# Kernel optimization log

Hardware: AMD Instinct MI355X
Metric: run time of the kernel (lower is better)

The kernel has to match this reference:

```python
import jax, jax.numpy as jnp
import numpy as np


def _apply_rope(x, cos, sin):
    # x: [B, h, T, d]; cos/sin: [T, d//2]
    B, h, T, d = x.shape
    xp = x.astype(jnp.float32).reshape(B, h, T, d // 2, 2)
    xr, xi = xp[..., 0], xp[..., 1]
    c = cos[None, None]  # [1,1,T,d//2]
    s = sin[None, None]
    out_r = xr * c - xi * s
    out_i = xr * s + xi * c
    out = jnp.stack([out_r, out_i], axis=-1).reshape(B, h, T, d)
    return out.astype(x.dtype)


def setup_inputs() -> dict:
    key = jax.random.key(0)
    ks = jax.random.split(key, 7)
    B, T, C = 1, 4096, 1024
    h = 16
    d = C // h
    return {
        "x": jax.random.normal(ks[0], (B, T, C), jnp.float32),
        "freqs_cos": jax.random.normal(ks[1], (T, d // 2), jnp.float32),
        "freqs_sin": jax.random.normal(ks[2], (T, d // 2), jnp.float32),
        "Wq": jax.random.normal(ks[3], (C, C), jnp.float32) * 0.02,
        "Wk": jax.random.normal(ks[4], (C, C), jnp.float32) * 0.02,
        "Wv": jax.random.normal(ks[5], (C, C), jnp.float32) * 0.02,
        "Wo": jax.random.normal(ks[6], (C, C), jnp.float32) * 0.02,
    }


def reference(x, freqs_cos, freqs_sin, Wq, Wk, Wv, Wo):
    B, T, C = x.shape
    h = 16
    d = C // h
    # nn.Linear(bias=False): y = x @ W^T, W is [out, in]
    q = jnp.einsum("btc,oc->bto", x, Wq).reshape(B, T, h, d).transpose(0, 2, 1, 3)
    k = jnp.einsum("btc,oc->bto", x, Wk).reshape(B, T, h, d).transpose(0, 2, 1, 3)
    v = jnp.einsum("btc,oc->bto", x, Wv).reshape(B, T, h, d).transpose(0, 2, 1, 3)
    q = _apply_rope(q, freqs_cos, freqs_sin)
    k = _apply_rope(k, freqs_cos, freqs_sin)
    scale = 1.0 / jnp.sqrt(jnp.asarray(d, x.dtype))
    scores = jnp.einsum("bhqd,bhkd->bhqk", q, k) * scale  # [B,h,T,T]
    causal = jnp.tril(jnp.ones((T, T), bool))
    scores = jnp.where(causal[None, None], scores, -jnp.inf)
    att = jax.nn.softmax(scores.astype(jnp.float32), axis=-1).astype(q.dtype)
    y = jnp.einsum("bhqk,bhkd->bhqd", att, v)
    y = y.transpose(0, 2, 1, 3).reshape(B, T, C)
    return jnp.einsum("btc,oc->bto", y, Wo)  # dropout p=0 (eval)
```

## Files before the change

### kernel.cpp

```cpp
#include <hip/hip_runtime.h>
#include <hip/hip_bf16.h>
#include <math.h>

#define TT 4096
#define CC 1024
#define NH 16
#define HD 64

typedef unsigned short ushortT;
typedef __attribute__((ext_vector_type(8))) short short8;
typedef __attribute__((ext_vector_type(4))) float f32x4;

#define GLOAD_LDS16(gp, lp)                                                   \
    __builtin_amdgcn_global_load_lds(                                         \
        (const __attribute__((address_space(1))) void*)(gp),                  \
        (__attribute__((address_space(3))) void*)(lp), 16, 0, 0)

#define EXP2F(x) __builtin_amdgcn_exp2f(x)

__device__ __forceinline__ ushortT f2bf(float f) {
    __hip_bfloat16 h = __float2bfloat16(f);
    ushortT u; __builtin_memcpy(&u, &h, 2); return u;
}
__device__ __forceinline__ float bf2f(ushortT u) {
    return __uint_as_float(((unsigned)u) << 16);
}

#define PSLOT_BYTES 17408
#define NCHUNK_H 62
#define NTICK (NCHUNK_H * NH)

__global__ __launch_bounds__(256) void cvt_all(
    const float* __restrict__ x,  const float* __restrict__ wq,
    const float* __restrict__ wk, const float* __restrict__ wv,
    const float* __restrict__ wo,
    ushortT* __restrict__ xb,  ushortT* __restrict__ wqb,
    ushortT* __restrict__ wkb, ushortT* __restrict__ wvb,
    ushortT* __restrict__ wob)
{
    const int i = (blockIdx.x * 256 + threadIdx.x) * 4;
    const int NX = TT * CC, NW = CC * CC;
    const float* s; ushortT* d; int off;
    if (i < NX)               { s = x;  d = xb;  off = i; }
    else if (i < NX + NW)     { s = wq; d = wqb; off = i - NX; }
    else if (i < NX + 2 * NW) { s = wk; d = wkb; off = i - NX - NW; }
    else if (i < NX + 3 * NW) { s = wv; d = wvb; off = i - NX - 2 * NW; }
    else                      { s = wo; d = wob; off = i - NX - 3 * NW; }
    float4 v = *(const float4*)(s + off);
    *(ushort4*)(d + off) = make_ushort4(f2bf(v.x), f2bf(v.y), f2bf(v.z), f2bf(v.w));
}

__global__ __launch_bounds__(256) void gemm_qkv(
    const ushortT* __restrict__ A,
    const ushortT* __restrict__ Bq, const ushortT* __restrict__ Bk,
    const ushortT* __restrict__ Bv,
    const float* __restrict__ fcos, const float* __restrict__ fsin,
    ushortT* __restrict__ q16, ushortT* __restrict__ k16,
    ushortT* __restrict__ vt16)
{
    __shared__ char lds[49152];

    const int z = blockIdx.z;
    const ushortT* B = (z == 0) ? Bq : (z == 1) ? Bk : Bv;

    const int lin = (int)(blockIdx.y * gridDim.x + blockIdx.x);
    const int nwg8 = (int)((gridDim.x * gridDim.y) >> 3);
    const int swz = (lin & 7) * nwg8 + (lin >> 3);
    const int bm = (swz % (int)gridDim.x) * 128;
    const int bn = (swz / (int)gridDim.x) * 128;
    const int tid = threadIdx.x;
    const int w = tid >> 6, l = tid & 63;
    const int wm = w >> 1, wn = w & 1;

    f32x4 acc[4][4] = {};

    auto stageg = [&](int kk, int base) {
        #pragma unroll
        for (int e = 0; e < 2; ++e) {
            const int D = (w * 2 + e) * 1024 + l * 16;
            const int r = D >> 6;
            const int c = (D & 63) >> 1;
            GLOAD_LDS16(A + (size_t)(bm + r) * CC + kk + c, lds + base + (w * 2 + e) * 1024);
            GLOAD_LDS16(B + (size_t)(bn + r) * CC + kk + c, lds + base + 8192 + (w * 2 + e) * 1024);
        }
    };

    stageg(0, 0);
    stageg(32, 16384);

    for (int kt = 0; kt < 32; ++kt) {
        const int cur = kt % 3;
        if (kt + 2 < 32) {
            stageg((kt + 2) * 32, ((kt + 2) % 3) * 16384);
            asm volatile("s_waitcnt vmcnt(8)" ::: "memory");
        } else if (kt + 1 < 32) {
            asm volatile("s_waitcnt vmcnt(4)" ::: "memory");
        } else {
            asm volatile("s_waitcnt vmcnt(0)" ::: "memory");
        }
        __builtin_amdgcn_s_barrier();
        __builtin_amdgcn_sched_barrier(0);

        const ushortT* As = (const ushortT*)(lds + cur * 16384);
        const ushortT* Bs = (const ushortT*)(lds + cur * 16384 + 8192);

        short8 af[4], bfr[4];
        #pragma unroll
        for (int i = 0; i < 4; ++i) {
            int row = wm * 64 + i * 16 + (l & 15);
            af[i] = *(const short8*)(As + row * 32 + (l >> 4) * 8);
        }
        #pragma unroll
        for (int j = 0; j < 4; ++j) {
            int row = wn * 64 + j * 16 + (l & 15);
            bfr[j] = *(const short8*)(Bs + row * 32 + (l >> 4) * 8);
        }
        #pragma unroll
        for (int i = 0; i < 4; ++i)
            #pragma unroll
            for (int j = 0; j < 4; ++j)
                acc[i][j] = __builtin_amdgcn_mfma_f32_16x16x32_bf16(af[i], bfr[j], acc[i][j], 0, 0, 0);
        __builtin_amdgcn_s_barrier();
    }

    if (z < 2) {
        const float rsc = (z == 0) ? 0.18033688011112042f : 1.0f;
        ushortT* dq = (z == 0) ? q16 : k16;
        float* cs = (float*)lds;
        float* sn = (float*)(lds + 16384);
        for (int idx = tid; idx < 128 * 32; idx += 256) {
            int rr = idx >> 5, cc2 = idx & 31;
            cs[idx] = fcos[(size_t)(bm + rr) * 32 + cc2];
            sn[idx] = fsin[(size_t)(bm + rr) * 32 + cc2];
        }
        __syncthreads();
        #pragma unroll
        for (int i = 0; i < 4; ++i)
            #pragma unroll
            for (int j = 0; j < 4; ++j)
                #pragma unroll
                for (int r = 0; r < 4; ++r) {
                    const int lt = wm * 64 + i * 16 + (l >> 4) * 4 + r;
                    const int o = bn + wn * 64 + j * 16 + (l & 15);
                    const float v = acc[i][j][r];
                    const float p = __shfl_xor(v, 1);
                    const int pp = (o & 63) >> 1;
                    const float cv = cs[lt * 32 + pp], sv = sn[lt * 32 + pp];
                    const float outv = ((o & 1) ? (p * sv + v * cv) : (v * cv - p * sv)) * rsc;
                    const int t = bm + lt, head = o >> 6, dd = o & 63;
                    dq[((size_t)head * TT + t) * HD + dd] = f2bf(outv);
                }
    } else {
        #pragma unroll
        for (int i = 0; i < 4; ++i)
            #pragma unroll
            for (int j = 0; j < 4; ++j)
                #pragma unroll
                for (int r = 0; r < 4; ++r) {
                    const int t = bm + wm * 64 + i * 16 + (l >> 4) * 4 + r;
                    const int o = bn + wn * 64 + j * 16 + (l & 15);
                    const int head = o >> 6, dd = o & 63;
                    const int k = t & 63;
                    const int slot = (k & 32) | (((k >> 2) & 3) << 3)
                                   | (((k >> 4) & 1) << 2) | (k & 3);
                    vt16[((size_t)(head * HD + dd)) * TT + (t & ~63) + slot] = f2bf(acc[i][j][r]);
                }
    }
}

__global__ __launch_bounds__(256) void gemm_out(
    const ushortT* __restrict__ A, const ushortT* __restrict__ B,
    float* __restrict__ dout)
{
    __shared__ char lds[49152];

    const int lin = (int)(blockIdx.y * gridDim.x + blockIdx.x);
    const int nwg8 = (int)((gridDim.x * gridDim.y) >> 3);
    const int swz = (lin & 7) * nwg8 + (lin >> 3);
    const int bm = (swz % (int)gridDim.x) * 128;
    const int bn = (swz / (int)gridDim.x) * 128;
    const int tid = threadIdx.x;
    const int w = tid >> 6, l = tid & 63;
    const int wm = w >> 1, wn = w & 1;

    f32x4 acc[4][4] = {};

    auto stageg = [&](int kk, int base) {
        #pragma unroll
        for (int e = 0; e < 2; ++e) {
            const int D = (w * 2 + e) * 1024 + l * 16;
            const int r = D >> 6;
            const int c = (D & 63) >> 1;
            GLOAD_LDS16(A + (size_t)(bm + r) * CC + kk + c, lds + base + (w * 2 + e) * 1024);
            GLOAD_LDS16(B + (size_t)(bn + r) * CC + kk + c, lds + base + 8192 + (w * 2 + e) * 1024);
        }
    };

    stageg(0, 0);
    stageg(32, 16384);

    for (int kt = 0; kt < 32; ++kt) {
        const int cur = kt % 3;
        if (kt + 2 < 32) {
            stageg((kt + 2) * 32, ((kt + 2) % 3) * 16384);
            asm volatile("s_waitcnt vmcnt(8)" ::: "memory");
        } else if (kt + 1 < 32) {
            asm volatile("s_waitcnt vmcnt(4)" ::: "memory");
        } else {
            asm volatile("s_waitcnt vmcnt(0)" ::: "memory");
        }
        __builtin_amdgcn_s_barrier();
        __builtin_amdgcn_sched_barrier(0);

        const ushortT* As = (const ushortT*)(lds + cur * 16384);
        const ushortT* Bs = (const ushortT*)(lds + cur * 16384 + 8192);

        short8 af[4], bfr[4];
        #pragma unroll
        for (int i = 0; i < 4; ++i) {
            int row = wm * 64 + i * 16 + (l & 15);
            af[i] = *(const short8*)(As + row * 32 + (l >> 4) * 8);
        }
        #pragma unroll
        for (int j = 0; j < 4; ++j) {
            int row = wn * 64 + j * 16 + (l & 15);
            bfr[j] = *(const short8*)(Bs + row * 32 + (l >> 4) * 8);
        }
        #pragma unroll
        for (int i = 0; i < 4; ++i)
            #pragma unroll
            for (int j = 0; j < 4; ++j)
                acc[i][j] = __builtin_amdgcn_mfma_f32_16x16x32_bf16(af[i], bfr[j], acc[i][j], 0, 0, 0);
        __builtin_amdgcn_s_barrier();
    }

    #pragma unroll
    for (int i = 0; i < 4; ++i)
        #pragma unroll
        for (int j = 0; j < 4; ++j)
            #pragma unroll
            for (int r = 0; r < 4; ++r) {
                const int t = bm + wm * 64 + i * 16 + (l >> 4) * 4 + r;
                const int o = bn + wn * 64 + j * 16 + (l & 15);
                dout[(size_t)t * CC + o] = acc[i][j][r];
            }
}

__global__ __launch_bounds__(512) void attn_mfma(
    const ushortT* __restrict__ q16, const ushortT* __restrict__ k16,
    const ushortT* __restrict__ vt16, ushortT* __restrict__ y16,
    char* __restrict__ parts, int* __restrict__ counter)
{
    const int tid = threadIdx.x;
    const int w = tid >> 6, l = tid & 63;
    const int g = l >> 4, q = l & 15;

    __shared__ char lds[32768];

    for (;;) {
        if (tid == 0) {
            int tk0 = atomicAdd(counter, 1);
            *(int*)lds = tk0;
        }
        __syncthreads();
        const int tk = *(const int*)lds;
        __syncthreads();
        if (tk >= NTICK) break;

        const int head = tk / NCHUNK_H;
        const int t = tk - head * NCHUNK_H;
        int qc, ci, nsplit;
        if (t < 27)      { qc = 31 - t / 3; ci = t % 3; nsplit = 3; }
        else if (t < 51) { int u = t - 27; qc = 22 - u / 2; ci = u & 1; nsplit = 2; }
        else             { qc = 10 - (t - 51); ci = -1; nsplit = 1; }
        const int ntl = 2 * qc + 2;
        const int kb0 = (ci <= 0) ? 0 : ci * ntl / nsplit;
        const int kb1 = (ci < 0) ? (ntl - 1) : ((ci + 1) * ntl / nsplit - 1);

        const int rowbase = qc * 128 + w * 16;
        const int qrow = rowbase + q;
        short8 qa[2];
        {
            const ushortT* qp = q16 + ((size_t)head * TT + qrow) * HD + g * 8;
            qa[0] = *(const short8*)(qp);
            qa[1] = *(const short8*)(qp + 32);
        }

        f32x4 yacc[4] = {};
        float m_s = -1e30f, l_s = 0.0f;

        auto stage = [&](int kb, int base) {
            #pragma unroll
            for (int e = 0; e < 2; ++e) {
                const int seg = w * 2 + e;
                const int D = seg * 1024 + l * 16;
                if (seg < 8) {
                    const int row = D >> 7;
                    const int src = D ^ ((row & 7) << 4);
                    const int col = (src & 127) >> 1;
                    GLOAD_LDS16(k16 + ((size_t)head * TT + (size_t)kb * 64 + row) * HD + col,
                                lds + base + seg * 1024);
                } else {
                    const int Dv = D - 8192;
                    const int row = Dv >> 7;
                    const int src = Dv ^ ((row & 7) << 4);
                    const int col = (src & 127) >> 1;
                    GLOAD_LDS16(vt16 + ((size_t)head * HD + row) * TT + (size_t)kb * 64 + col,
                                lds + base + seg * 1024);
                }
            }
        };

        int cur = 0;
        stage(kb0, 0);

        for (int kb = kb0; kb <= kb1; ++kb) {
            if (kb + 1 <= kb1) {
                stage(kb + 1, (cur ^ 1) * 16384);
                asm volatile("s_waitcnt vmcnt(2)" ::: "memory");
            } else {
                asm volatile("s_waitcnt vmcnt(0)" ::: "memory");
            }
            __builtin_amdgcn_s_barrier();
            __builtin_amdgcn_sched_barrier(0);

            const bool skip = (kb * 64 > rowbase + 15);
            if (!skip) {
                const char* Ks  = lds + cur * 16384;
                const char* Vts = Ks + 8192;

                f32x4 s[4] = {};
                __builtin_amdgcn_s_setprio(1);
                #pragma unroll
                for (int ks = 0; ks < 2; ++ks)
                    #pragma unroll
                    for (int kg = 0; kg < 4; ++kg) {
                        const int key = kg * 16 + q;
                        int b = key * 128 + ks * 64 + g * 16;
                        b ^= (key & 7) << 4;
                        short8 kf = *(const short8*)(Ks + b);
                        s[kg] = __builtin_amdgcn_mfma_f32_16x16x32_bf16(kf, qa[ks], s[kg], 0, 0, 0);
                    }
                __builtin_amdgcn_s_setprio(0);

                if (kb * 64 + 63 > rowbase) {
                    #pragma unroll
                    for (int kg = 0; kg < 4; ++kg)
                        #pragma unroll
                        for (int r = 0; r < 4; ++r)
                            if (kb * 64 + kg * 16 + 4 * g + r > qrow) s[kg][r] = -1e30f;
                }

                float ilmax = s[0][0];
                #pragma unroll
                for (int kg = 0; kg < 4; ++kg)
                    #pragma unroll
                    for (int r = 0; r < 4; ++r)
                        ilmax = fmaxf(ilmax, s[kg][r]);

                if (__any(ilmax > m_s + 8.0f)) {
                    float mx = ilmax;
                    mx = fmaxf(mx, __shfl_xor(mx, 16));
                    mx = fmaxf(mx, __shfl_xor(mx, 32));
                    const float mnew = fmaxf(m_s, mx);
                    const float al = EXP2F(m_s - mnew);
                    m_s = mnew;
                    l_s *= al;
                    float aly[4];
                    #pragma unroll
                    for (int r = 0; r < 4; ++r)
                        aly[r] = __shfl(al, 20 * g + r);
                    #pragma unroll
                    for (int dg = 0; dg < 4; ++dg)
                        #pragma unroll
                        for (int r = 0; r < 4; ++r)
                            yacc[dg][r] *= aly[r];
                }

                unsigned U[4], V[4];
                float ls = 0.0f;
                #pragma unroll
                for (int kg = 0; kg < 4; ++kg) {
                    const float p0 = EXP2F(s[kg][0] - m_s);
                    const float p1 = EXP2F(s[kg][1] - m_s);
                    const float p2 = EXP2F(s[kg][2] - m_s);
                    const float p3 = EXP2F(s[kg][3] - m_s);
                    ls += (p0 + p1) + (p2 + p3);
                    asm("v_cvt_pk_bf16_f32 %0, %1, %2" : "=v"(U[kg]) : "v"(p0), "v"(p1));
                    asm("v_cvt_pk_bf16_f32 %0, %1, %2" : "=v"(V[kg]) : "v"(p2), "v"(p3));
                }
                l_s += ls;

                __builtin_amdgcn_s_setprio(1);
                #pragma unroll
                for (int ks2 = 0; ks2 < 2; ++ks2) {
                    union { unsigned u[4]; short8 s8; } pu;
                    pu.u[0] = U[2 * ks2];     pu.u[1] = V[2 * ks2];
                    pu.u[2] = U[2 * ks2 + 1]; pu.u[3] = V[2 * ks2 + 1];
                    const short8 pa = pu.s8;
                    const char* Vts2 = Vts;
                    #pragma unroll
                    for (int dg = 0; dg < 4; ++dg) {
                        const int dd = dg * 16 + q;
                        int vb = dd * 128 + ks2 * 64 + g * 16;
                        vb ^= (dd & 7) << 4;
                        short8 vf = *(const short8*)(Vts2 + vb);
                        yacc[dg] = __builtin_amdgcn_mfma_f32_16x16x32_bf16(pa, vf, yacc[dg], 0, 0, 0);
                    }
                }
                __builtin_amdgcn_s_setprio(0);
            }
            __builtin_amdgcn_s_barrier();
            cur ^= 1;
        }

        l_s += __shfl_xor(l_s, 16);
        l_s += __shfl_xor(l_s, 32);
        float lr[4];
        #pragma unroll
        for (int r = 0; r < 4; ++r)
            lr[r] = __shfl(l_s, 20 * g + r);

        if (ci < 0) {
            #pragma unroll
            for (int r = 0; r < 4; ++r) lr[r] = 1.0f / lr[r];
            #pragma unroll
            for (int dg = 0; dg < 4; ++dg)
                #pragma unroll
                for (int r = 0; r < 4; ++r) {
                    const int trow = rowbase + 4 * g + r;
                    const int col = head * HD + dg * 16 + q;
                    y16[(size_t)trow * CC + col] = f2bf(yacc[dg][r] * lr[r]);
                }
        } else {
            float mr[4];
            #pragma unroll
            for (int r = 0; r < 4; ++r)
                mr[r] = __shfl(m_s, 20 * g + r);
            const int sidx = head * 51 +
                ((qc >= 23) ? (31 - qc) * 3 + ci : 27 + (22 - qc) * 2 + ci);
            char* pb = parts + (size_t)sidx * PSLOT_BYTES;
            ushortT* yp = (ushortT*)pb;
            float* mp = (float*)(pb + 16384);
            float* lp = (float*)(pb + 16896);
            #pragma unroll
            for (int dg = 0; dg < 4; ++dg)
                #pragma unroll
                for (int r = 0; r < 4; ++r) {
                    const int row = w * 16 + 4 * g + r;
                    yp[row * 64 + dg * 16 + q] = f2bf(yacc[dg][r]);
                }
            if (q == 0) {
                #pragma unroll
                for (int r = 0; r < 4; ++r) {
                    const int row = w * 16 + 4 * g + r;
                    mp[row] = mr[r];
                    lp[row] = lr[r];
                }
            }
        }
    }
}

__global__ __launch_bounds__(256) void attn_combine(
    const char* __restrict__ parts, ushortT* __restrict__ y16)
{
    const int qc = 11 + blockIdx.x;
    const int head = blockIdx.y;
    const int nsplit = (qc >= 23) ? 3 : 2;
    const int base = head * 51 + ((qc >= 23) ? (31 - qc) * 3 : 27 + (22 - qc) * 2);
    const int tid = threadIdx.x;

    #pragma unroll
    for (int pass = 0; pass < 4; ++pass) {
        const int idx = pass * 2048 + tid * 8;
        const int row = idx >> 6, col = idx & 63;

        float m_i[3], l_i[3];
        float M = -1e30f;
        for (int i = 0; i < nsplit; ++i) {
            const char* pb = parts + (size_t)(base + i) * PSLOT_BYTES;
            m_i[i] = *(const float*)(pb + 16384 + row * 4);
            l_i[i] = *(const float*)(pb + 16896 + row * 4);
            M = fmaxf(M, m_i[i]);
        }
        float wgt[3], L = 0.0f;
        for (int i = 0; i < nsplit; ++i) {
            wgt[i] = EXP2F(m_i[i] - M);
            L += l_i[i] * wgt[i];
        }
        const float Linv = 1.0f / L;

        float acc[8] = {};
        for (int i = 0; i < nsplit; ++i) {
            const ushortT* yp = (const ushortT*)(parts + (size_t)(base + i) * PSLOT_BYTES);
            short8 v = *(const short8*)(yp + row * 64 + col);
            #pragma unroll
            for (int j = 0; j < 8; ++j)
                acc[j] += bf2f((ushortT)v[j]) * wgt[i];
        }
        union { ushortT u[8]; short8 s8; } ov;
        #pragma unroll
        for (int j = 0; j < 8; ++j)
            ov.u[j] = f2bf(acc[j] * Linv);
        const int trow = qc * 128 + row;
        *(short8*)(&y16[(size_t)trow * CC + head * HD + col]) = ov.s8;
    }
}

extern "C" void kernel_launch(void* const* d_in, const int* in_sizes, int n_in,
                              void* d_out, int out_size, void* d_ws, size_t ws_size,
                              hipStream_t stream) {
    const float* x    = (const float*)d_in[0];
    const float* fcos = (const float*)d_in[1];
    const float* fsin = (const float*)d_in[2];
    const float* Wq   = (const float*)d_in[3];
    const float* Wk   = (const float*)d_in[4];
    const float* Wv   = (const float*)d_in[5];
    const float* Wo   = (const float*)d_in[6];
    float* out = (float*)d_out;

    char* ws = (char*)d_ws;
    ushortT* xb  = (ushortT*)(ws);
    ushortT* wqb = (ushortT*)(ws + (8u << 20));
    ushortT* wkb = (ushortT*)(ws + (10u << 20));
    ushortT* wvb = (ushortT*)(ws + (12u << 20));
    ushortT* wob = (ushortT*)(ws + (14u << 20));
    ushortT* q16 = (ushortT*)(ws + (16u << 20));
    ushortT* k16 = (ushortT*)(ws + (24u << 20));
    ushortT* vt16 = (ushortT*)(ws + (32u << 20));
    ushortT* y16 = (ushortT*)(ws + (40u << 20));
    char* parts = ws;
    int* counter = (int*)(ws + (14u << 20) - 16);

    cvt_all<<<(TT * CC + 4 * CC * CC) / 4 / 256, 256, 0, stream>>>(
        x, Wq, Wk, Wv, Wo, xb, wqb, wkb, wvb, wob);

    dim3 qkvgrid(TT / 128, CC / 128, 3);
    gemm_qkv<<<qkvgrid, 256, 0, stream>>>(xb, wqb, wkb, wvb, fcos, fsin,
                                          q16, k16, vt16);

    hipMemsetAsync(counter, 0, 4, stream);
    attn_mfma<<<1024, 512, 0, stream>>>(q16, k16, vt16, y16, parts, counter);

    dim3 cgrid(21, NH);
    attn_combine<<<cgrid, 256, 0, stream>>>(parts, y16);

    dim3 ggrid(TT / 128, CC / 128);
    gemm_out<<<ggrid, 256, 0, stream>>>(y16, wob, out);
}
```

Measured before the change: 143.5 us.

## Process two 16-row query tiles per wave to reuse K/V fragments

```diff
diff --git a/kernel.cpp b/kernel.cpp
--- a/kernel.cpp
+++ b/kernel.cpp
@@ -246,7 +246,7 @@
             }
 }
 
-__global__ __launch_bounds__(512) void attn_mfma(
+__global__ __launch_bounds__(256) void attn_mfma(
     const ushortT* __restrict__ q16, const ushortT* __restrict__ k16,
     const ushortT* __restrict__ vt16, ushortT* __restrict__ y16,
     char* __restrict__ parts, int* __restrict__ counter)
@@ -277,22 +277,26 @@
         const int kb0 = (ci <= 0) ? 0 : ci * ntl / nsplit;
         const int kb1 = (ci < 0) ? (ntl - 1) : ((ci + 1) * ntl / nsplit - 1);
 
-        const int rowbase = qc * 128 + w * 16;
-        const int qrow = rowbase + q;
-        short8 qa[2];
+        const int rowbase = qc * 128 + w * 32;
+        const int qrowA = rowbase + q;
+        const int qrowB = rowbase + 16 + q;
+        short8 qaA[2], qaB[2];
         {
-            const ushortT* qp = q16 + ((size_t)head * TT + qrow) * HD + g * 8;
-            qa[0] = *(const short8*)(qp);
-            qa[1] = *(const short8*)(qp + 32);
-        }
-
-        f32x4 yacc[4] = {};
-        float m_s = -1e30f, l_s = 0.0f;
+            const ushortT* qp = q16 + ((size_t)head * TT + qrowA) * HD + g * 8;
+            qaA[0] = *(const short8*)(qp);
+            qaA[1] = *(const short8*)(qp + 32);
+            const ushortT* qp2 = q16 + ((size_t)head * TT + qrowB) * HD + g * 8;
+            qaB[0] = *(const short8*)(qp2);
+            qaB[1] = *(const short8*)(qp2 + 32);
+        }
+
+        f32x4 yA[4] = {}, yB[4] = {};
+        float mA = -1e30f, lA = 0.0f, mB = -1e30f, lB = 0.0f;
 
         auto stage = [&](int kb, int base) {
             #pragma unroll
-            for (int e = 0; e < 2; ++e) {
-                const int seg = w * 2 + e;
+            for (int e = 0; e < 4; ++e) {
+                const int seg = w * 4 + e;
                 const int D = seg * 1024 + l * 16;
                 if (seg < 8) {
                     const int row = D >> 7;
@@ -317,19 +321,19 @@
         for (int kb = kb0; kb <= kb1; ++kb) {
             if (kb + 1 <= kb1) {
                 stage(kb + 1, (cur ^ 1) * 16384);
-                asm volatile("s_waitcnt vmcnt(2)" ::: "memory");
+                asm volatile("s_waitcnt vmcnt(4)" ::: "memory");
             } else {
                 asm volatile("s_waitcnt vmcnt(0)" ::: "memory");
             }
             __builtin_amdgcn_s_barrier();
             __builtin_amdgcn_sched_barrier(0);
 
-            const bool skip = (kb * 64 > rowbase + 15);
+            const bool skip = (kb * 64 > rowbase + 31);
             if (!skip) {
                 const char* Ks  = lds + cur * 16384;
                 const char* Vts = Ks + 8192;
 
-                f32x4 s[4] = {};
+                f32x4 sA[4] = {}, sB[4] = {};
                 __builtin_amdgcn_s_setprio(1);
                 #pragma unroll
                 for (int ks = 0; ks < 2; ++ks)
@@ -338,8 +342,9 @@
                         const int key = kg * 16 + q;
                         int b = key * 128 + ks * 64 + g * 16;
                         b ^= (key & 7) << 4;
-                        short8 kf = *(const short8*)(Ks + b);
-                        s[kg] = __builtin_amdgcn_mfma_f32_16x16x32_bf16(kf, qa[ks], s[kg], 0, 0, 0);
+                        const short8 kf = *(const short8*)(Ks + b);
+                        sA[kg] = __builtin_amdgcn_mfma_f32_16x16x32_bf16(kf, qaA[ks], sA[kg], 0, 0, 0);
+                        sB[kg] = __builtin_amdgcn_mfma_f32_16x16x32_bf16(kf, qaB[ks], sB[kg], 0, 0, 0);
                     }
                 __builtin_amdgcn_s_setprio(0);
 
@@ -347,25 +352,27 @@
                     #pragma unroll
                     for (int kg = 0; kg < 4; ++kg)
                         #pragma unroll
-                        for (int r = 0; r < 4; ++r)
-                            if (kb * 64 + kg * 16 + 4 * g + r > qrow) s[kg][r] = -1e30f;
-                }
-
-                float ilmax = s[0][0];
+                        for (int r = 0; r < 4; ++r) {
+                            const int key = kb * 64 + kg * 16 + 4 * g + r;
+                            if (key > qrowA) sA[kg][r] = -1e30f;
+                            if (key > qrowB) sB[kg][r] = -1e30f;
+                        }
+                }
+
+                float ilmax = sA[0][0];
                 #pragma unroll
                 for (int kg = 0; kg < 4; ++kg)
                     #pragma unroll
                     for (int r = 0; r < 4; ++r)
-                        ilmax = fmaxf(ilmax, s[kg][r]);
-
-                if (__any(ilmax > m_s + 8.0f)) {
+                        ilmax = fmaxf(ilmax, sA[kg][r]);
+                if (__any(ilmax > mA + 8.0f)) {
                     float mx = ilmax;
                     mx = fmaxf(mx, __shfl_xor(mx, 16));
                     mx = fmaxf(mx, __shfl_xor(mx, 32));
-                    const float mnew = fmaxf(m_s, mx);
-                    const float al = EXP2F(m_s - mnew);
-                    m_s = mnew;
-                    l_s *= al;
+                    const float mnew = fmaxf(mA, mx);
+                    const float al = EXP2F(mA - mnew);
+                    mA = mnew;
+                    lA *= al;
                     float aly[4];
                     #pragma unroll
                     for (int r = 0; r < 4; ++r)
@@ -374,38 +381,80 @@
                     for (int dg = 0; dg < 4; ++dg)
                         #pragma unroll
                         for (int r = 0; r < 4; ++r)
-                            yacc[dg][r] *= aly[r];
-                }
-
-                unsigned U[4], V[4];
-                float ls = 0.0f;
-                #pragma unroll
-                for (int kg = 0; kg < 4; ++kg) {
-                    const float p0 = EXP2F(s[kg][0] - m_s);
-                    const float p1 = EXP2F(s[kg][1] - m_s);
-                    const float p2 = EXP2F(s[kg][2] - m_s);
-                    const float p3 = EXP2F(s[kg][3] - m_s);
-                    ls += (p0 + p1) + (p2 + p3);
-                    asm("v_cvt_pk_bf16_f32 %0, %1, %2" : "=v"(U[kg]) : "v"(p0), "v"(p1));
-                    asm("v_cvt_pk_bf16_f32 %0, %1, %2" : "=v"(V[kg]) : "v"(p2), "v"(p3));
-                }
-                l_s += ls;
+                            yA[dg][r] *= aly[r];
+                }
+                unsigned UA[4], VA[4];
+                {
+                    float ls = 0.0f;
+                    #pragma unroll
+                    for (int kg = 0; kg < 4; ++kg) {
+                        const float p0 = EXP2F(sA[kg][0] - mA);
+                        const float p1 = EXP2F(sA[kg][1] - mA);
+                        const float p2 = EXP2F(sA[kg][2] - mA);
+                        const float p3 = EXP2F(sA[kg][3] - mA);
+                        ls += (p0 + p1) + (p2 + p3);
+                        asm("v_cvt_pk_bf16_f32 %0, %1, %2" : "=v"(UA[kg]) : "v"(p0), "v"(p1));
+                        asm("v_cvt_pk_bf16_f32 %0, %1, %2" : "=v"(VA[kg]) : "v"(p2), "v"(p3));
+                    }
+                    lA += ls;
+                }
+
+                float ilmaxB = sB[0][0];
+                #pragma unroll
+                for (int kg = 0; kg < 4; ++kg)
+                    #pragma unroll
+                    for (int r = 0; r < 4; ++r)
+                        ilmaxB = fmaxf(ilmaxB, sB[kg][r]);
+                if (__any(ilmaxB > mB + 8.0f)) {
+                    float mx = ilmaxB;
+                    mx = fmaxf(mx, __shfl_xor(mx, 16));
+                    mx = fmaxf(mx, __shfl_xor(mx, 32));
+                    const float mnew = fmaxf(mB, mx);
+                    const float al = EXP2F(mB - mnew);
+                    mB = mnew;
+                    lB *= al;
+                    float aly[4];
+                    #pragma unroll
+                    for (int r = 0; r < 4; ++r)
+                        aly[r] = __shfl(al, 20 * g + r);
+                    #pragma unroll
+                    for (int dg = 0; dg < 4; ++dg)
+                        #pragma unroll
+                        for (int r = 0; r < 4; ++r)
+                            yB[dg][r] *= aly[r];
+                }
+                unsigned UB[4], VB[4];
+                {
+                    float ls = 0.0f;
+                    #pragma unroll
+                    for (int kg = 0; kg < 4; ++kg) {
+                        const float p0 = EXP2F(sB[kg][0] - mB);
+                        const float p1 = EXP2F(sB[kg][1] - mB);
+                        const float p2 = EXP2F(sB[kg][2] - mB);
+                        const float p3 = EXP2F(sB[kg][3] - mB);
+                        ls += (p0 + p1) + (p2 + p3);
+                        asm("v_cvt_pk_bf16_f32 %0, %1, %2" : "=v"(UB[kg]) : "v"(p0), "v"(p1));
+                        asm("v_cvt_pk_bf16_f32 %0, %1, %2" : "=v"(VB[kg]) : "v"(p2), "v"(p3));
+                    }
+                    lB += ls;
+                }
 
                 __builtin_amdgcn_s_setprio(1);
                 #pragma unroll
                 for (int ks2 = 0; ks2 < 2; ++ks2) {
-                    union { unsigned u[4]; short8 s8; } pu;
-                    pu.u[0] = U[2 * ks2];     pu.u[1] = V[2 * ks2];
-                    pu.u[2] = U[2 * ks2 + 1]; pu.u[3] = V[2 * ks2 + 1];
-                    const short8 pa = pu.s8;
-                    const char* Vts2 = Vts;
+                    union { unsigned u[4]; short8 s8; } pa, pb;
+                    pa.u[0] = UA[2 * ks2];     pa.u[1] = VA[2 * ks2];
+                    pa.u[2] = UA[2 * ks2 + 1]; pa.u[3] = VA[2 * ks2 + 1];
+                    pb.u[0] = UB[2 * ks2];     pb.u[1] = VB[2 * ks2];
+                    pb.u[2] = UB[2 * ks2 + 1]; pb.u[3] = VB[2 * ks2 + 1];
                     #pragma unroll
                     for (int dg = 0; dg < 4; ++dg) {
                         const int dd = dg * 16 + q;
                         int vb = dd * 128 + ks2 * 64 + g * 16;
                         vb ^= (dd & 7) << 4;
-                        short8 vf = *(const short8*)(Vts2 + vb);
-                        yacc[dg] = __builtin_amdgcn_mfma_f32_16x16x32_bf16(pa, vf, yacc[dg], 0, 0, 0);
+                        const short8 vf = *(const short8*)(Vts + vb);
+                        yA[dg] = __builtin_amdgcn_mfma_f32_16x16x32_bf16(pa.s8, vf, yA[dg], 0, 0, 0);
+                        yB[dg] = __builtin_amdgcn_mfma_f32_16x16x32_bf16(pb.s8, vf, yB[dg], 0, 0, 0);
                     }
                 }
                 __builtin_amdgcn_s_setprio(0);
@@ -414,29 +463,37 @@
             cur ^= 1;
         }
 
-        l_s += __shfl_xor(l_s, 16);
-        l_s += __shfl_xor(l_s, 32);
-        float lr[4];
-        #pragma unroll
-        for (int r = 0; r < 4; ++r)
-            lr[r] = __shfl(l_s, 20 * g + r);
+        lA += __shfl_xor(lA, 16);
+        lA += __shfl_xor(lA, 32);
+        lB += __shfl_xor(lB, 16);
+        lB += __shfl_xor(lB, 32);
+        float lrA[4], lrB[4];
+        #pragma unroll
+        for (int r = 0; r < 4; ++r) {
+            lrA[r] = __shfl(lA, 20 * g + r);
+            lrB[r] = __shfl(lB, 20 * g + r);
+        }
 
         if (ci < 0) {
             #pragma unroll
-            for (int r = 0; r < 4; ++r) lr[r] = 1.0f / lr[r];
+            for (int r = 0; r < 4; ++r) { lrA[r] = 1.0f / lrA[r]; lrB[r] = 1.0f / lrB[r]; }
             #pragma unroll
             for (int dg = 0; dg < 4; ++dg)
                 #pragma unroll
                 for (int r = 0; r < 4; ++r) {
-                    const int trow = rowbase + 4 * g + r;
                     const int col = head * HD + dg * 16 + q;
-                    y16[(size_t)trow * CC + col] = f2bf(yacc[dg][r] * lr[r]);
+                    const int trA = rowbase + 4 * g + r;
+                    const int trB = rowbase + 16 + 4 * g + r;
+                    y16[(size_t)trA * CC + col] = f2bf(yA[dg][r] * lrA[r]);
+                    y16[(size_t)trB * CC + col] = f2bf(yB[dg][r] * lrB[r]);
                 }
         } else {
-            float mr[4];
-            #pragma unroll
-            for (int r = 0; r < 4; ++r)
-                mr[r] = __shfl(m_s, 20 * g + r);
+            float mrA[4], mrB[4];
+            #pragma unroll
+            for (int r = 0; r < 4; ++r) {
+                mrA[r] = __shfl(mA, 20 * g + r);
+                mrB[r] = __shfl(mB, 20 * g + r);
+            }
             const int sidx = head * 51 +
                 ((qc >= 23) ? (31 - qc) * 3 + ci : 27 + (22 - qc) * 2 + ci);
             char* pb = parts + (size_t)sidx * PSLOT_BYTES;
@@ -447,15 +504,18 @@
             for (int dg = 0; dg < 4; ++dg)
                 #pragma unroll
                 for (int r = 0; r < 4; ++r) {
-                    const int row = w * 16 + 4 * g + r;
-                    yp[row * 64 + dg * 16 + q] = f2bf(yacc[dg][r]);
+                    const int rowA = w * 32 + 4 * g + r;
+                    const int rowB = w * 32 + 16 + 4 * g + r;
+                    yp[rowA * 64 + dg * 16 + q] = f2bf(yA[dg][r]);
+                    yp[rowB * 64 + dg * 16 + q] = f2bf(yB[dg][r]);
                 }
             if (q == 0) {
                 #pragma unroll
                 for (int r = 0; r < 4; ++r) {
-                    const int row = w * 16 + 4 * g + r;
-                    mp[row] = mr[r];
-                    lp[row] = lr[r];
+                    const int rowA = w * 32 + 4 * g + r;
+                    const int rowB = w * 32 + 16 + 4 * g + r;
+                    mp[rowA] = mrA[r];  lp[rowA] = lrA[r];
+                    mp[rowB] = mrB[r];  lp[rowB] = lrB[r];
                 }
             }
         }
@@ -541,7 +601,7 @@
                                           q16, k16, vt16);
 
     hipMemsetAsync(counter, 0, 4, stream);
-    attn_mfma<<<1024, 512, 0, stream>>>(q16, k16, vt16, y16, parts, counter);
+    attn_mfma<<<1024, 256, 0, stream>>>(q16, k16, vt16, y16, parts, counter);
 
     dim3 cgrid(21, NH);
     attn_combine<<<cgrid, 256, 0, stream>>>(parts, y16);
```

After: 193.3 us. 1.35x slower.

## Switch attention to 32x32x16 MFMA with 4 waves of 32 query rows

Applied to the files above, without the earlier changes.

```diff
diff --git a/kernel.cpp b/kernel.cpp
--- a/kernel.cpp
+++ b/kernel.cpp
@@ -10,6 +10,7 @@
 typedef unsigned short ushortT;
 typedef __attribute__((ext_vector_type(8))) short short8;
 typedef __attribute__((ext_vector_type(4))) float f32x4;
+typedef __attribute__((ext_vector_type(16))) float f32x16;
 
 #define GLOAD_LDS16(gp, lp)                                                   \
     __builtin_amdgcn_global_load_lds(                                         \
@@ -161,8 +162,7 @@
                     const int o = bn + wn * 64 + j * 16 + (l & 15);
                     const int head = o >> 6, dd = o & 63;
                     const int k = t & 63;
-                    const int slot = (k & 32) | (((k >> 2) & 3) << 3)
-                                   | (((k >> 4) & 1) << 2) | (k & 3);
+                    const int slot = (k & 51) | ((k & 4) << 1) | ((k & 8) >> 1);
                     vt16[((size_t)(head * HD + dd)) * TT + (t & ~63) + slot] = f2bf(acc[i][j][r]);
                 }
     }
@@ -246,14 +246,14 @@
             }
 }
 
-__global__ __launch_bounds__(512) void attn_mfma(
+__global__ __launch_bounds__(256) void attn_mfma(
     const ushortT* __restrict__ q16, const ushortT* __restrict__ k16,
     const ushortT* __restrict__ vt16, ushortT* __restrict__ y16,
     char* __restrict__ parts, int* __restrict__ counter)
 {
     const int tid = threadIdx.x;
     const int w = tid >> 6, l = tid & 63;
-    const int g = l >> 4, q = l & 15;
+    const int hi = l >> 5, q = l & 31;
 
     __shared__ char lds[32768];
 
@@ -277,22 +277,25 @@
         const int kb0 = (ci <= 0) ? 0 : ci * ntl / nsplit;
         const int kb1 = (ci < 0) ? (ntl - 1) : ((ci + 1) * ntl / nsplit - 1);
 
-        const int rowbase = qc * 128 + w * 16;
+        const int rowbase = qc * 128 + w * 32;
         const int qrow = rowbase + q;
-        short8 qa[2];
+
+        short8 qa[4];
         {
-            const ushortT* qp = q16 + ((size_t)head * TT + qrow) * HD + g * 8;
+            const ushortT* qp = q16 + ((size_t)head * TT + qrow) * HD + hi * 8;
             qa[0] = *(const short8*)(qp);
-            qa[1] = *(const short8*)(qp + 32);
-        }
-
-        f32x4 yacc[4] = {};
+            qa[1] = *(const short8*)(qp + 16);
+            qa[2] = *(const short8*)(qp + 32);
+            qa[3] = *(const short8*)(qp + 48);
+        }
+
+        f32x16 y0 = {}, y1 = {};
         float m_s = -1e30f, l_s = 0.0f;
 
         auto stage = [&](int kb, int base) {
             #pragma unroll
-            for (int e = 0; e < 2; ++e) {
-                const int seg = w * 2 + e;
+            for (int e = 0; e < 4; ++e) {
+                const int seg = w * 4 + e;
                 const int D = seg * 1024 + l * 16;
                 if (seg < 8) {
                     const int row = D >> 7;
@@ -317,96 +320,84 @@
         for (int kb = kb0; kb <= kb1; ++kb) {
             if (kb + 1 <= kb1) {
                 stage(kb + 1, (cur ^ 1) * 16384);
-                asm volatile("s_waitcnt vmcnt(2)" ::: "memory");
+                asm volatile("s_waitcnt vmcnt(4)" ::: "memory");
             } else {
                 asm volatile("s_waitcnt vmcnt(0)" ::: "memory");
             }
             __builtin_amdgcn_s_barrier();
             __builtin_amdgcn_sched_barrier(0);
 
-            const bool skip = (kb * 64 > rowbase + 15);
+            const bool skip = (kb * 64 > rowbase + 31);
             if (!skip) {
                 const char* Ks  = lds + cur * 16384;
                 const char* Vts = Ks + 8192;
 
-                f32x4 s[4] = {};
+                f32x16 s0 = {}, s1 = {};
                 __builtin_amdgcn_s_setprio(1);
                 #pragma unroll
-                for (int ks = 0; ks < 2; ++ks)
-                    #pragma unroll
-                    for (int kg = 0; kg < 4; ++kg) {
-                        const int key = kg * 16 + q;
-                        int b = key * 128 + ks * 64 + g * 16;
-                        b ^= (key & 7) << 4;
-                        short8 kf = *(const short8*)(Ks + b);
-                        s[kg] = __builtin_amdgcn_mfma_f32_16x16x32_bf16(kf, qa[ks], s[kg], 0, 0, 0);
-                    }
+                for (int c = 0; c < 4; ++c) {
+                    int b0 = q * 128 + c * 32 + hi * 16;
+                    b0 ^= (q & 7) << 4;
+                    const short8 kf0 = *(const short8*)(Ks + b0);
+                    const short8 kf1 = *(const short8*)(Ks + b0 + 4096);
+                    s0 = __builtin_amdgcn_mfma_f32_32x32x16_bf16(kf0, qa[c], s0, 0, 0, 0);
+                    s1 = __builtin_amdgcn_mfma_f32_32x32x16_bf16(kf1, qa[c], s1, 0, 0, 0);
+                }
                 __builtin_amdgcn_s_setprio(0);
 
                 if (kb * 64 + 63 > rowbase) {
                     #pragma unroll
-                    for (int kg = 0; kg < 4; ++kg)
-                        #pragma unroll
-                        for (int r = 0; r < 4; ++r)
-                            if (kb * 64 + kg * 16 + 4 * g + r > qrow) s[kg][r] = -1e30f;
-                }
-
-                float ilmax = s[0][0];
-                #pragma unroll
-                for (int kg = 0; kg < 4; ++kg)
-                    #pragma unroll
-                    for (int r = 0; r < 4; ++r)
-                        ilmax = fmaxf(ilmax, s[kg][r]);
+                    for (int reg = 0; reg < 16; ++reg) {
+                        const int key = kb * 64 + (reg & 3) + 8 * (reg >> 2) + 4 * hi;
+                        if (key > qrow) s0[reg] = -1e30f;
+                        if (key + 32 > qrow) s1[reg] = -1e30f;
+                    }
+                }
+
+                float ilmax = s0[0];
+                #pragma unroll
+                for (int reg = 1; reg < 16; ++reg) ilmax = fmaxf(ilmax, s0[reg]);
+                #pragma unroll
+                for (int reg = 0; reg < 16; ++reg) ilmax = fmaxf(ilmax, s1[reg]);
 
                 if (__any(ilmax > m_s + 8.0f)) {
-                    float mx = ilmax;
-                    mx = fmaxf(mx, __shfl_xor(mx, 16));
-                    mx = fmaxf(mx, __shfl_xor(mx, 32));
+                    const float mx = fmaxf(ilmax, __shfl_xor(ilmax, 32));
                     const float mnew = fmaxf(m_s, mx);
                     const float al = EXP2F(m_s - mnew);
                     m_s = mnew;
                     l_s *= al;
-                    float aly[4];
                     #pragma unroll
-                    for (int r = 0; r < 4; ++r)
-                        aly[r] = __shfl(al, 20 * g + r);
-                    #pragma unroll
-                    for (int dg = 0; dg < 4; ++dg)
-                        #pragma unroll
-                        for (int r = 0; r < 4; ++r)
-                            yacc[dg][r] *= aly[r];
-                }
-
-                unsigned U[4], V[4];
+                    for (int reg = 0; reg < 16; ++reg) { y0[reg] *= al; y1[reg] *= al; }
+                }
+
+                unsigned pk0[8], pk1[8];
                 float ls = 0.0f;
                 #pragma unroll
-                for (int kg = 0; kg < 4; ++kg) {
-                    const float p0 = EXP2F(s[kg][0] - m_s);
-                    const float p1 = EXP2F(s[kg][1] - m_s);
-                    const float p2 = EXP2F(s[kg][2] - m_s);
-                    const float p3 = EXP2F(s[kg][3] - m_s);
-                    ls += (p0 + p1) + (p2 + p3);
-                    asm("v_cvt_pk_bf16_f32 %0, %1, %2" : "=v"(U[kg]) : "v"(p0), "v"(p1));
-                    asm("v_cvt_pk_bf16_f32 %0, %1, %2" : "=v"(V[kg]) : "v"(p2), "v"(p3));
+                for (int v = 0; v < 8; ++v) {
+                    const float a0 = EXP2F(s0[2 * v] - m_s);
+                    const float a1 = EXP2F(s0[2 * v + 1] - m_s);
+                    const float b0f = EXP2F(s1[2 * v] - m_s);
+                    const float b1f = EXP2F(s1[2 * v + 1] - m_s);
+                    ls += (a0 + a1) + (b0f + b1f);
+                    asm("v_cvt_pk_bf16_f32 %0, %1, %2" : "=v"(pk0[v]) : "v"(a0), "v"(a1));
+                    asm("v_cvt_pk_bf16_f32 %0, %1, %2" : "=v"(pk1[v]) : "v"(b0f), "v"(b1f));
                 }
                 l_s += ls;
 
                 __builtin_amdgcn_s_setprio(1);
                 #pragma unroll
-                for (int ks2 = 0; ks2 < 2; ++ks2) {
-                    union { unsigned u[4]; short8 s8; } pu;
-                    pu.u[0] = U[2 * ks2];     pu.u[1] = V[2 * ks2];
-                    pu.u[2] = U[2 * ks2 + 1]; pu.u[3] = V[2 * ks2 + 1];
-                    const short8 pa = pu.s8;
-                    const char* Vts2 = Vts;
-                    #pragma unroll
-                    for (int dg = 0; dg < 4; ++dg) {
-                        const int dd = dg * 16 + q;
-                        int vb = dd * 128 + ks2 * 64 + g * 16;
-                        vb ^= (dd & 7) << 4;
-                        short8 vf = *(const short8*)(Vts2 + vb);
-                        yacc[dg] = __builtin_amdgcn_mfma_f32_16x16x32_bf16(pa, vf, yacc[dg], 0, 0, 0);
-                    }
+                for (int c = 0; c < 4; ++c) {
+                    union { unsigned u[4]; short8 s8; } pb;
+                    if (c == 0)      { pb.u[0] = pk0[0]; pb.u[1] = pk0[1]; pb.u[2] = pk0[2]; pb.u[3] = pk0[3]; }
+                    else if (c == 1) { pb.u[0] = pk0[4]; pb.u[1] = pk0[5]; pb.u[2] = pk0[6]; pb.u[3] = pk0[7]; }
+                    else if (c == 2) { pb.u[0] = pk1[0]; pb.u[1] = pk1[1]; pb.u[2] = pk1[2]; pb.u[3] = pk1[3]; }
+                    else             { pb.u[0] = pk1[4]; pb.u[1] = pk1[5]; pb.u[2] = pk1[6]; pb.u[3] = pk1[7]; }
+                    int vb = q * 128 + c * 32 + hi * 16;
+                    vb ^= (q & 7) << 4;
+                    const short8 vf0 = *(const short8*)(Vts + vb);
+                    const short8 vf1 = *(const short8*)(Vts + vb + 4096);
+                    y0 = __builtin_amdgcn_mfma_f32_32x32x16_bf16(vf0, pb.s8, y0, 0, 0, 0);
+                    y1 = __builtin_amdgcn_mfma_f32_32x32x16_bf16(vf1, pb.s8, y1, 0, 0, 0);
                 }
                 __builtin_amdgcn_s_setprio(0);
             }
@@ -414,49 +405,34 @@
             cur ^= 1;
         }
 
-        l_s += __shfl_xor(l_s, 16);
         l_s += __shfl_xor(l_s, 32);
-        float lr[4];
-        #pragma unroll
-        for (int r = 0; r < 4; ++r)
-            lr[r] = __shfl(l_s, 20 * g + r);
 
         if (ci < 0) {
-            #pragma unroll
-            for (int r = 0; r < 4; ++r) lr[r] = 1.0f / lr[r];
-            #pragma unroll
-            for (int dg = 0; dg < 4; ++dg)
-                #pragma unroll
-                for (int r = 0; r < 4; ++r) {
-                    const int trow = rowbase + 4 * g + r;
-                    const int col = head * HD + dg * 16 + q;
-                    y16[(size_t)trow * CC + col] = f2bf(yacc[dg][r] * lr[r]);
-                }
+            const float linv = 1.0f / l_s;
+            #pragma unroll
+            for (int reg = 0; reg < 16; ++reg) {
+                const int d = (reg & 3) + 8 * (reg >> 2) + 4 * hi;
+                const size_t rb = (size_t)qrow * CC + head * HD;
+                y16[rb + d]      = f2bf(y0[reg] * linv);
+                y16[rb + d + 32] = f2bf(y1[reg] * linv);
+            }
         } else {
-            float mr[4];
-            #pragma unroll
-            for (int r = 0; r < 4; ++r)
-                mr[r] = __shfl(m_s, 20 * g + r);
             const int sidx = head * 51 +
                 ((qc >= 23) ? (31 - qc) * 3 + ci : 27 + (22 - qc) * 2 + ci);
             char* pb = parts + (size_t)sidx * PSLOT_BYTES;
             ushortT* yp = (ushortT*)pb;
             float* mp = (float*)(pb + 16384);
             float* lp = (float*)(pb + 16896);
-            #pragma unroll
-            for (int dg = 0; dg < 4; ++dg)
-                #pragma unroll
-                for (int r = 0; r < 4; ++r) {
-                    const int row = w * 16 + 4 * g + r;
-                    yp[row * 64 + dg * 16 + q] = f2bf(yacc[dg][r]);
-                }
-            if (q == 0) {
-                #pragma unroll
-                for (int r = 0; r < 4; ++r) {
-                    const int row = w * 16 + 4 * g + r;
-                    mp[row] = mr[r];
-                    lp[row] = lr[r];
-                }
+            const int row = w * 32 + q;
+            #pragma unroll
+            for (int reg = 0; reg < 16; ++reg) {
+                const int d = (reg & 3) + 8 * (reg >> 2) + 4 * hi;
+                yp[row * 64 + d]      = f2bf(y0[reg]);
+                yp[row * 64 + d + 32] = f2bf(y1[reg]);
+            }
+            if (hi == 0) {
+                mp[row] = m_s;
+                lp[row] = l_s;
             }
         }
     }
@@ -541,7 +517,7 @@
                                           q16, k16, vt16);
 
     hipMemsetAsync(counter, 0, 4, stream);
-    attn_mfma<<<1024, 512, 0, stream>>>(q16, k16, vt16, y16, parts, counter);
+    attn_mfma<<<1024, 256, 0, stream>>>(q16, k16, vt16, y16, parts, counter);
 
     dim3 cgrid(21, NH);
     attn_combine<<<cgrid, 256, 0, stream>>>(parts, y16);
```

After: 156.5 us. 1.09x slower.

## Fuse split-KV combine into attention kernel via completion counters; raise MFMA priority in GEMMs

Applied to the files above, without the earlier changes.

```diff
diff --git a/kernel.cpp b/kernel.cpp
--- a/kernel.cpp
+++ b/kernel.cpp
@@ -115,11 +115,13 @@
             int row = wn * 64 + j * 16 + (l & 15);
             bfr[j] = *(const short8*)(Bs + row * 32 + (l >> 4) * 8);
         }
+        __builtin_amdgcn_s_setprio(1);
         #pragma unroll
         for (int i = 0; i < 4; ++i)
             #pragma unroll
             for (int j = 0; j < 4; ++j)
                 acc[i][j] = __builtin_amdgcn_mfma_f32_16x16x32_bf16(af[i], bfr[j], acc[i][j], 0, 0, 0);
+        __builtin_amdgcn_s_setprio(0);
         __builtin_amdgcn_s_barrier();
     }
 
@@ -226,11 +228,13 @@
             int row = wn * 64 + j * 16 + (l & 15);
             bfr[j] = *(const short8*)(Bs + row * 32 + (l >> 4) * 8);
         }
+        __builtin_amdgcn_s_setprio(1);
         #pragma unroll
         for (int i = 0; i < 4; ++i)
             #pragma unroll
             for (int j = 0; j < 4; ++j)
                 acc[i][j] = __builtin_amdgcn_mfma_f32_16x16x32_bf16(af[i], bfr[j], acc[i][j], 0, 0, 0);
+        __builtin_amdgcn_s_setprio(0);
         __builtin_amdgcn_s_barrier();
     }
 
@@ -249,7 +253,7 @@
 __global__ __launch_bounds__(512) void attn_mfma(
     const ushortT* __restrict__ q16, const ushortT* __restrict__ k16,
     const ushortT* __restrict__ vt16, ushortT* __restrict__ y16,
-    char* __restrict__ parts, int* __restrict__ counter)
+    char* __restrict__ parts, int* __restrict__ done, int* __restrict__ counter)
 {
     const int tid = threadIdx.x;
     const int w = tid >> 6, l = tid & 63;
@@ -398,13 +402,12 @@
                     pu.u[0] = U[2 * ks2];     pu.u[1] = V[2 * ks2];
                     pu.u[2] = U[2 * ks2 + 1]; pu.u[3] = V[2 * ks2 + 1];
                     const short8 pa = pu.s8;
-                    const char* Vts2 = Vts;
                     #pragma unroll
                     for (int dg = 0; dg < 4; ++dg) {
                         const int dd = dg * 16 + q;
                         int vb = dd * 128 + ks2 * 64 + g * 16;
                         vb ^= (dd & 7) << 4;
-                        short8 vf = *(const short8*)(Vts2 + vb);
+                        short8 vf = *(const short8*)(Vts + vb);
                         yacc[dg] = __builtin_amdgcn_mfma_f32_16x16x32_bf16(pa, vf, yacc[dg], 0, 0, 0);
                     }
                 }
@@ -437,9 +440,9 @@
             #pragma unroll
             for (int r = 0; r < 4; ++r)
                 mr[r] = __shfl(m_s, 20 * g + r);
-            const int sidx = head * 51 +
-                ((qc >= 23) ? (31 - qc) * 3 + ci : 27 + (22 - qc) * 2 + ci);
-            char* pb = parts + (size_t)sidx * PSLOT_BYTES;
+            const int sbase = head * 51 +
+                ((qc >= 23) ? (31 - qc) * 3 : 27 + (22 - qc) * 2);
+            char* pb = parts + (size_t)(sbase + ci) * PSLOT_BYTES;
             ushortT* yp = (ushortT*)pb;
             float* mp = (float*)(pb + 16384);
             float* lp = (float*)(pb + 16896);
@@ -458,53 +461,49 @@
                     lp[row] = lr[r];
                 }
             }
-        }
-    }
-}
-
-__global__ __launch_bounds__(256) void attn_combine(
-    const char* __restrict__ parts, ushortT* __restrict__ y16)
-{
-    const int qc = 11 + blockIdx.x;
-    const int head = blockIdx.y;
-    const int nsplit = (qc >= 23) ? 3 : 2;
-    const int base = head * 51 + ((qc >= 23) ? (31 - qc) * 3 : 27 + (22 - qc) * 2);
-    const int tid = threadIdx.x;
-
-    #pragma unroll
-    for (int pass = 0; pass < 4; ++pass) {
-        const int idx = pass * 2048 + tid * 8;
-        const int row = idx >> 6, col = idx & 63;
-
-        float m_i[3], l_i[3];
-        float M = -1e30f;
-        for (int i = 0; i < nsplit; ++i) {
-            const char* pb = parts + (size_t)(base + i) * PSLOT_BYTES;
-            m_i[i] = *(const float*)(pb + 16384 + row * 4);
-            l_i[i] = *(const float*)(pb + 16896 + row * 4);
-            M = fmaxf(M, m_i[i]);
-        }
-        float wgt[3], L = 0.0f;
-        for (int i = 0; i < nsplit; ++i) {
-            wgt[i] = EXP2F(m_i[i] - M);
-            L += l_i[i] * wgt[i];
-        }
-        const float Linv = 1.0f / L;
-
-        float acc[8] = {};
-        for (int i = 0; i < nsplit; ++i) {
-            const ushortT* yp = (const ushortT*)(parts + (size_t)(base + i) * PSLOT_BYTES);
-            short8 v = *(const short8*)(yp + row * 64 + col);
-            #pragma unroll
-            for (int j = 0; j < 8; ++j)
-                acc[j] += bf2f((ushortT)v[j]) * wgt[i];
-        }
-        union { ushortT u[8]; short8 s8; } ov;
-        #pragma unroll
-        for (int j = 0; j < 8; ++j)
-            ov.u[j] = f2bf(acc[j] * Linv);
-        const int trow = qc * 128 + row;
-        *(short8*)(&y16[(size_t)trow * CC + head * HD + col]) = ov.s8;
+
+            __threadfence();
+            __syncthreads();
+            if (tid == 0)
+                *(int*)lds = atomicAdd(&done[head * 21 + (qc - 11)], 1);
+            __syncthreads();
+            const int prev = *(const int*)lds;
+            __syncthreads();
+            if (prev == nsplit - 1) {
+                __threadfence();
+                #pragma unroll
+                for (int pass = 0; pass < 2; ++pass) {
+                    const int idx = (pass * 512 + tid) * 8;
+                    const int row = idx >> 6, col = idx & 63;
+                    float m_i[3], l_i[3];
+                    float M = -1e30f;
+                    for (int i = 0; i < nsplit; ++i) {
+                        const char* p2 = parts + (size_t)(sbase + i) * PSLOT_BYTES;
+                        m_i[i] = *(const float*)(p2 + 16384 + row * 4);
+                        l_i[i] = *(const float*)(p2 + 16896 + row * 4);
+                        M = fmaxf(M, m_i[i]);
+                    }
+                    float L = 0.0f;
+                    float acc8[8] = {};
+                    for (int i = 0; i < nsplit; ++i) {
+                        const float wgt = EXP2F(m_i[i] - M);
+                        L += l_i[i] * wgt;
+                        const ushortT* yp2 = (const ushortT*)(parts + (size_t)(sbase + i) * PSLOT_BYTES);
+                        short8 v = *(const short8*)(yp2 + row * 64 + col);
+                        #pragma unroll
+                        for (int j = 0; j < 8; ++j)
+                            acc8[j] += bf2f((ushortT)v[j]) * wgt;
+                    }
+                    const float Linv = 1.0f / L;
+                    union { ushortT u[8]; short8 s8; } ov;
+                    #pragma unroll
+                    for (int j = 0; j < 8; ++j)
+                        ov.u[j] = f2bf(acc8[j] * Linv);
+                    const int trow = qc * 128 + row;
+                    *(short8*)(&y16[(size_t)trow * CC + head * HD + col]) = ov.s8;
+                }
+            }
+        }
     }
 }
 
@@ -531,6 +530,8 @@
     ushortT* vt16 = (ushortT*)(ws + (32u << 20));
     ushortT* y16 = (ushortT*)(ws + (40u << 20));
     char* parts = ws;
+    char* syncpage = ws + (14u << 20) - 4096;
+    int* done = (int*)syncpage;
     int* counter = (int*)(ws + (14u << 20) - 16);
 
     cvt_all<<<(TT * CC + 4 * CC * CC) / 4 / 256, 256, 0, stream>>>(
@@ -540,11 +541,8 @@
     gemm_qkv<<<qkvgrid, 256, 0, stream>>>(xb, wqb, wkb, wvb, fcos, fsin,
                                           q16, k16, vt16);
 
-    hipMemsetAsync(counter, 0, 4, stream);
-    attn_mfma<<<1024, 512, 0, stream>>>(q16, k16, vt16, y16, parts, counter);
-
-    dim3 cgrid(21, NH);
-    attn_combine<<<cgrid, 256, 0, stream>>>(parts, y16);
+    hipMemsetAsync(syncpage, 0, 4096, stream);
+    attn_mfma<<<1024, 512, 0, stream>>>(q16, k16, vt16, y16, parts, done, counter);
 
     dim3 ggrid(TT / 128, CC / 128);
     gemm_out<<<ggrid, 256, 0, stream>>>(y16, wob, out);
```

After: 420.0 us. +192.7%, slower.
